# Performance work log

Hardware: AMD Instinct MI355X
Metric: run time of the kernel (lower is better)

Reference implementation:

```python
import jax, jax.numpy as jnp
import numpy as np

B, T, I, H = 64, 1024, 256, 512


def setup_inputs() -> dict:
    key = jax.random.key(0)
    ks = jax.random.split(key, 5)
    s = 1.0 / np.sqrt(H)  # PyTorch LSTM init scale (uniform(-s, s)); we use scaled normal
    return {
        "x": jax.random.normal(ks[0], (B, T, I), dtype=jnp.float32),
        "w_ih": jax.random.normal(ks[1], (4 * H, I), dtype=jnp.float32) * s,
        "w_hh": jax.random.normal(ks[2], (4 * H, H), dtype=jnp.float32) * s,
        "b_ih": jax.random.normal(ks[3], (4 * H,), dtype=jnp.float32) * s,
        "b_hh": jax.random.normal(ks[4], (4 * H,), dtype=jnp.float32) * s,
    }


def _lstm(x, w_ih, w_hh, b_ih, b_hh):
    # x: [B, T, I]. Precompute input projections for all timesteps at once.
    pre = jnp.einsum("bti,gi->btg", x, w_ih) + b_ih + b_hh  # [B, T, 4H]
    pre = jnp.swapaxes(pre, 0, 1)  # [T, B, 4H] for scan over time

    h0 = jnp.zeros((x.shape[0], H), dtype=x.dtype)
    c0 = jnp.zeros((x.shape[0], H), dtype=x.dtype)

    def step(carry, pre_t):
        h, c = carry
        gates = pre_t + h @ w_hh.T  # [B, 4H]
        i, f, g, o = jnp.split(gates, 4, axis=-1)  # PyTorch gate order: i, f, g, o
        i = jax.nn.sigmoid(i)
        f = jax.nn.sigmoid(f)
        g = jnp.tanh(g)
        o = jax.nn.sigmoid(o)
        c = f * c + i * g
        h = o * jnp.tanh(c)
        return (h, c), h

    (h_n, c_n), hs = jax.lax.scan(step, (h0, c0), pre)
    out = jnp.swapaxes(hs, 0, 1)  # [B, T, H] (batch_first=True)
    return out, (h_n[None], c_n[None])  # h_n/c_n: [num_layers=1, B, H]


def reference(x, w_ih, w_hh, b_ih, b_hh):
    return _lstm(x, w_ih, w_hh, b_ih, b_hh)
```

## Files before the change

### kernel.cpp

```cpp
#include <hip/hip_runtime.h>
#include <cstdint>
#include <cstddef>


#define NBATCH 64
#define TSTEPS 1024
#define IDIM   256
#define HDIM   512
#define WS     776
#define ABUF_USHORT (16 * WS)
#define BIAS_OFF    (2 * ABUF_USHORT * 2)
#define SMEM_BYTES  (BIAS_OFF + 1024)

#define HB_WORDS 32768

typedef __attribute__((ext_vector_type(8))) short short8x;
typedef __attribute__((ext_vector_type(4))) float f32x4;
typedef __attribute__((ext_vector_type(4))) unsigned int u32x4;

__device__ __forceinline__ float sigmoid_f(float v) {
    float e = __builtin_amdgcn_exp2f(v * -1.442695040888963f);
    return __builtin_amdgcn_rcpf(1.0f + e);
}
__device__ __forceinline__ float tanh_f(float v) {
    float e = __builtin_amdgcn_exp2f(v * 2.885390081777927f);
    return 1.0f - 2.0f * __builtin_amdgcn_rcpf(e + 1.0f);
}
__device__ __forceinline__ unsigned short f2bf(float f) {
    unsigned int u = __float_as_uint(f);
    return (unsigned short)((u + 0x7fffu + ((u >> 16) & 1u)) >> 16);
}
__device__ __forceinline__ unsigned long long pack4(float4 v) {
    unsigned long long b0 = f2bf(v.x), b1 = f2bf(v.y), b2 = f2bf(v.z), b3 = f2bf(v.w);
    return b0 | (b1 << 16) | (b2 << 32) | (b3 << 48);
}
__device__ __forceinline__ unsigned int cvtpk_bf16(float a, float b) {
    unsigned int r;
    asm("v_cvt_pk_bf16_f32 %0, %1, %2" : "=v"(r) : "v"(a), "v"(b));
    return r;
}
__device__ __forceinline__ unsigned int pklo(unsigned int a, unsigned int b) {
    return (a & 0xffffu) | (b << 16);
}
__device__ __forceinline__ float bf_lo(unsigned int w) { return __uint_as_float(w << 16); }
__device__ __forceinline__ float bf_hi(unsigned int w) { return __uint_as_float(w & 0xffff0000u); }

__global__ void __launch_bounds__(256, 1) lstm_persistent(
    const float* __restrict__ x,
    const float* __restrict__ w_ih,
    const float* __restrict__ w_hh,
    const float* __restrict__ b_ih,
    const float* __restrict__ b_hh,
    float* __restrict__ out,
    unsigned int* __restrict__ h_tb)
{
    const int tid = threadIdx.x;
    const int wg  = blockIdx.x;
    const int bg  = wg >> 3;
    const int hg  = wg & 7;

    extern __shared__ char smem[];
    unsigned short* a0 = (unsigned short*)smem;
    unsigned short* a1 = a0 + ABUF_USHORT;
    float* bias_s = (float*)(smem + BIAS_OFF);

    const int wv   = tid >> 6;
    const int lane = tid & 63;
    const int ln   = lane & 15;
    const int q    = lane >> 4;

    short8x af0[24], af1[24], af2[24], af3[24];
    {
        const int grb = (ln & 3) * HDIM + hg * 64 + wv * 16 + (ln >> 2) * 4;
#define LOADW(AF, TAU)                                                        \
        {                                                                     \
            const int gr = grb + (TAU);                                       \
            _Pragma("unroll")                                                 \
            for (int s = 0; s < 24; ++s) {                                    \
                const float* src = (s < 8)                                    \
                    ? (w_ih + (size_t)gr * IDIM + (s * 32 + q * 8))           \
                    : (w_hh + (size_t)gr * HDIM + ((s - 8) * 32 + q * 8));    \
                float4 v0 = *(const float4*)(src);                            \
                float4 v1 = *(const float4*)(src + 4);                        \
                union { short8x v; unsigned long long u[2]; } tmp;            \
                tmp.u[0] = pack4(v0);                                         \
                tmp.u[1] = pack4(v1);                                         \
                AF[s] = tmp.v;                                                \
            }                                                                 \
        }
        LOADW(af0, 0) LOADW(af1, 1) LOADW(af2, 2) LOADW(af3, 3)
#undef LOADW
    }

    if (ln < 4) {
        const int tau = ln;
        const int hid = hg * 64 + wv * 16 + q * 4 + tau;
        #pragma unroll
        for (int j = 0; j < 4; ++j)
            bias_s[(wv * 4 + q) * 16 + tau * 4 + j] =
                b_ih[j * HDIM + hid] + b_hh[j * HDIM + hid];
    }

    const int sn  = tid >> 4;
    const int sj  = tid & 15;
    const int gbn = bg * 16 + sn;
    const float* xbase = x + (size_t)gbn * TSTEPS * IDIM + sj * 16;

    const size_t hb_off = (size_t)(bg * 16 + ln) * HDIM + hg * 64 + wv * 16 + q * 4;
    float c0 = 0.f, c1 = 0.f, c2 = 0.f, c3 = 0.f;
    float hf0 = 0.f, hf1 = 0.f, hf2 = 0.f, hf3 = 0.f;

    for (int t = 0; t < TSTEPS; ++t) {
        unsigned short* abuf  = (t & 1) ? a1 : a0;
        unsigned short* axp   = abuf + sn * WS + sj * 16;
        unsigned int*   ahp32 = (unsigned int*)(abuf + sn * WS + IDIM + sj * 32);

        const float* xp = xbase + (size_t)t * IDIM;
        f32x4 xv0, xv1, xv2, xv3;
        asm volatile("global_load_dwordx4 %0, %1, off"           : "=v"(xv0) : "v"(xp));
        asm volatile("global_load_dwordx4 %0, %1, off offset:16" : "=v"(xv1) : "v"(xp));
        asm volatile("global_load_dwordx4 %0, %1, off offset:32" : "=v"(xv2) : "v"(xp));
        asm volatile("global_load_dwordx4 %0, %1, off offset:48" : "=v"(xv3) : "v"(xp));

        if (t > 0) {
            const unsigned int* hp =
                h_tb + (size_t)(t & 1) * HB_WORDS + (size_t)gbn * HDIM + sj * 32;
            u32x4 hv[8];
            const unsigned int tagw = (unsigned int)t << 16;
            unsigned pend = 0xffu;
            while (pend) {
#define POLL1(U, OFF)                                                         \
                if (pend & (1u << U))                                         \
                    asm volatile("global_load_dwordx4 %0, %1, off offset:" OFF \
                                 " sc0 sc1"                                   \
                                 : "=v"(hv[U]) : "v"(hp) : "memory");
                POLL1(0, "0")  POLL1(1, "16") POLL1(2, "32") POLL1(3, "48")
                POLL1(4, "64") POLL1(5, "80") POLL1(6, "96") POLL1(7, "112")
#undef POLL1
                asm volatile("s_waitcnt vmcnt(0)" ::: "memory");
                __builtin_amdgcn_sched_barrier(0);
                unsigned np = 0;
                #pragma unroll
                for (int u = 0; u < 8; ++u) {
                    if (pend & (1u << u)) {
                        unsigned m = ((hv[u][0] ^ tagw) | (hv[u][1] ^ tagw) |
                                      (hv[u][2] ^ tagw) | (hv[u][3] ^ tagw))
                                     & 0xffff0000u;
                        if (m) np |= (1u << u);
                    }
                }
                pend = np;
            }
            #pragma unroll
            for (int v = 0; v < 4; ++v) {
                u32x4 a = hv[2 * v], b = hv[2 * v + 1];
                u32x4 w4;
                w4[0] = pklo(a[0], a[1]);
                w4[1] = pklo(a[2], a[3]);
                w4[2] = pklo(b[0], b[1]);
                w4[3] = pklo(b[2], b[3]);
                *(u32x4*)(ahp32 + 4 * v) = w4;
            }
        } else {
            u32x4 z = {0u, 0u, 0u, 0u};
            #pragma unroll
            for (int v = 0; v < 4; ++v) *(u32x4*)(ahp32 + 4 * v) = z;
        }

        asm volatile("s_waitcnt vmcnt(0)" ::: "memory");
        __builtin_amdgcn_sched_barrier(0);
        {
            unsigned int* axp32 = (unsigned int*)axp;
            u32x4 xa, xb;
            xa[0] = cvtpk_bf16(xv0[0], xv0[1]);
            xa[1] = cvtpk_bf16(xv0[2], xv0[3]);
            xa[2] = cvtpk_bf16(xv1[0], xv1[1]);
            xa[3] = cvtpk_bf16(xv1[2], xv1[3]);
            xb[0] = cvtpk_bf16(xv2[0], xv2[1]);
            xb[1] = cvtpk_bf16(xv2[2], xv2[3]);
            xb[2] = cvtpk_bf16(xv3[0], xv3[1]);
            xb[3] = cvtpk_bf16(xv3[2], xv3[3]);
            *(u32x4*)(axp32)     = xa;
            *(u32x4*)(axp32 + 4) = xb;
        }
        __syncthreads();

        const unsigned short* Bbase = abuf + (size_t)ln * WS + q * 8;
        f32x4 ac0 = {0.f, 0.f, 0.f, 0.f};
        f32x4 ac1 = {0.f, 0.f, 0.f, 0.f};
        f32x4 ac2 = {0.f, 0.f, 0.f, 0.f};
        f32x4 ac3 = {0.f, 0.f, 0.f, 0.f};
        #pragma unroll
        for (int s = 0; s < 24; ++s) {
            short8x bf = *(const short8x*)(Bbase + s * 32);
            ac0 = __builtin_amdgcn_mfma_f32_16x16x32_bf16(af0[s], bf, ac0, 0, 0, 0);
            ac1 = __builtin_amdgcn_mfma_f32_16x16x32_bf16(af1[s], bf, ac1, 0, 0, 0);
            ac2 = __builtin_amdgcn_mfma_f32_16x16x32_bf16(af2[s], bf, ac2, 0, 0, 0);
            ac3 = __builtin_amdgcn_mfma_f32_16x16x32_bf16(af3[s], bf, ac3, 0, 0, 0);
        }

        const unsigned int tagw1 = (unsigned int)(t + 1) << 16;
        const float* bsl = bias_s + (wv * 4 + q) * 16;
        u32x4 pub;
#define ACT(ACC, TAU, CREF, HREF)                                             \
        {                                                                     \
            f32x4 bs = *(const f32x4*)(bsl + (TAU) * 4);                      \
            float ig = sigmoid_f(ACC[0] + bs[0]);                             \
            float fg = sigmoid_f(ACC[1] + bs[1]);                             \
            float gt = tanh_f   (ACC[2] + bs[2]);                             \
            float og = sigmoid_f(ACC[3] + bs[3]);                             \
            CREF = fg * CREF + ig * gt;                                       \
            HREF = og * tanh_f(CREF);                                         \
            pub[TAU] = tagw1 | (cvtpk_bf16(HREF, HREF) & 0xffffu);            \
        }
        ACT(ac0, 0, c0, hf0)
        ACT(ac1, 1, c1, hf1)
        ACT(ac2, 2, c2, hf2)
        ACT(ac3, 3, c3, hf3)
#undef ACT
        {
            unsigned int* hb = h_tb + (size_t)((t + 1) & 1) * HB_WORDS + hb_off;
            asm volatile("global_store_dwordx4 %0, %1, off sc0 sc1"
                         :: "v"(hb), "v"(pub) : "memory");
        }

        if (t > 0 && (sn & 7) == ((hg + t) & 7)) {
            float* op = out + ((size_t)gbn * TSTEPS + (t - 1)) * HDIM + sj * 32;
            #pragma unroll
            for (int v = 0; v < 4; ++v) {
                u32x4 w4 = *(const u32x4*)(ahp32 + 4 * v);
                f32x4 o0, o1;
                o0[0] = bf_lo(w4[0]); o0[1] = bf_hi(w4[0]);
                o0[2] = bf_lo(w4[1]); o0[3] = bf_hi(w4[1]);
                o1[0] = bf_lo(w4[2]); o1[1] = bf_hi(w4[2]);
                o1[2] = bf_lo(w4[3]); o1[3] = bf_hi(w4[3]);
                __builtin_nontemporal_store(o0, (f32x4*)(op + 8 * v));
                __builtin_nontemporal_store(o1, (f32x4*)(op + 8 * v + 4));
            }
        }
    }

    {
        const size_t HN_OFF = (size_t)NBATCH * TSTEPS * HDIM;
        const size_t CN_OFF = HN_OFF + (size_t)NBATCH * HDIM;
        const int gb   = bg * 16 + ln;
        const int hid0 = hg * 64 + wv * 16 + q * 4;
        f32x4 hv4 = {hf0, hf1, hf2, hf3};
        f32x4 cv4 = {c0, c1, c2, c3};
        *(f32x4*)(out + ((size_t)gb * TSTEPS + (TSTEPS - 1)) * HDIM + hid0) = hv4;
        *(f32x4*)(out + HN_OFF + (size_t)gb * HDIM + hid0) = hv4;
        *(f32x4*)(out + CN_OFF + (size_t)gb * HDIM + hid0) = cv4;
    }
}

extern "C" void kernel_launch(void* const* d_in, const int* in_sizes, int n_in,
                              void* d_out, int out_size, void* d_ws, size_t ws_size,
                              hipStream_t stream) {
    const float* x    = (const float*)d_in[0];
    const float* w_ih = (const float*)d_in[1];
    const float* w_hh = (const float*)d_in[2];
    const float* b_ih = (const float*)d_in[3];
    const float* b_hh = (const float*)d_in[4];
    float* out = (float*)d_out;

    unsigned int* h_tb = (unsigned int*)d_ws;

    (void)hipFuncSetAttribute((const void*)lstm_persistent,
                        hipFuncAttributeMaxDynamicSharedMemorySize, SMEM_BYTES);

    void* args[] = {(void*)&x, (void*)&w_ih, (void*)&w_hh, (void*)&b_ih,
                    (void*)&b_hh, (void*)&out, (void*)&h_tb};
    hipError_t err = hipLaunchCooperativeKernel((void*)lstm_persistent,
                                                dim3(32), dim3(256), args,
                                                SMEM_BYTES, stream);
    if (err != hipSuccess) {
        hipLaunchKernelGGL(lstm_persistent, dim3(32), dim3(256), SMEM_BYTES,
                           stream, x, w_ih, w_hh, b_ih, b_hh, out, h_tb);
    }
}
```

Before: 5.142 ms.

## Overlap input-projection MFMAs with hidden-state polling in persistent LSTM

Restructures each timestep so the x-projection part of the GEMM (first 8 K-slices) runs before the kernel has finished waiting for all of the previous step's hidden state from other workgroups. Hidden-state chunks that are already tagged valid are staged into LDS right away. Only the chunks that are still pending are re-polled after the x MFMAs, and a second barrier follows. This is meant to hide cross-workgroup synchronisation latency behind compute, at the cost of an extra __syncthreads per step and more complex polling control flow.

```diff
diff --git a/kernel.cpp b/kernel.cpp
--- a/kernel.cpp
+++ b/kernel.cpp
@@ -60,8 +60,8 @@
     const int hg  = wg & 7;
 
     extern __shared__ char smem[];
-    unsigned short* a0 = (unsigned short*)smem;
-    unsigned short* a1 = a0 + ABUF_USHORT;
+    unsigned short* a0s = (unsigned short*)smem;
+    unsigned short* a1s = a0s + ABUF_USHORT;
     float* bias_s = (float*)(smem + BIAS_OFF);
 
     const int wv   = tid >> 6;
@@ -111,7 +111,7 @@
     float hf0 = 0.f, hf1 = 0.f, hf2 = 0.f, hf3 = 0.f;
 
     for (int t = 0; t < TSTEPS; ++t) {
-        unsigned short* abuf  = (t & 1) ? a1 : a0;
+        unsigned short* abuf  = (t & 1) ? a1s : a0s;
         unsigned short* axp   = abuf + sn * WS + sj * 16;
         unsigned int*   ahp32 = (unsigned int*)(abuf + sn * WS + IDIM + sj * 32);
 
@@ -122,67 +122,78 @@
         asm volatile("global_load_dwordx4 %0, %1, off offset:32" : "=v"(xv2) : "v"(xp));
         asm volatile("global_load_dwordx4 %0, %1, off offset:48" : "=v"(xv3) : "v"(xp));
 
+        unsigned pend = 0;
+        u32x4 hv[8];
+        const unsigned int tagw = (unsigned int)t << 16;
+        const unsigned int* hp =
+            h_tb + (size_t)(t & 1) * HB_WORDS + (size_t)gbn * HDIM + sj * 32;
+
+#define POLL1(U, OFF)                                                         \
+        if (pend & (1u << U))                                                 \
+            asm volatile("global_load_dwordx4 %0, %1, off offset:" OFF        \
+                         " sc0 sc1"                                           \
+                         : "=v"(hv[U]) : "v"(hp) : "memory");
+#define CHECKSTAGE(U)                                                         \
+        if (pend & (1u << U)) {                                               \
+            unsigned m = ((hv[U][0] ^ tagw) | (hv[U][1] ^ tagw) |             \
+                          (hv[U][2] ^ tagw) | (hv[U][3] ^ tagw))              \
+                         & 0xffff0000u;                                       \
+            if (!m) {                                                         \
+                unsigned int p0 = pklo(hv[U][0], hv[U][1]);                   \
+                unsigned int p1 = pklo(hv[U][2], hv[U][3]);                   \
+                unsigned long long pw = (unsigned long long)p0                \
+                                      | ((unsigned long long)p1 << 32);       \
+                *(unsigned long long*)(ahp32 + 2 * (U)) = pw;                 \
+                pend &= ~(1u << U);                                           \
+            }                                                                 \
+        }
+
         if (t > 0) {
-            const unsigned int* hp =
-                h_tb + (size_t)(t & 1) * HB_WORDS + (size_t)gbn * HDIM + sj * 32;
-            u32x4 hv[8];
-            const unsigned int tagw = (unsigned int)t << 16;
-            unsigned pend = 0xffu;
-            while (pend) {
-#define POLL1(U, OFF)                                                         \
-                if (pend & (1u << U))                                         \
-                    asm volatile("global_load_dwordx4 %0, %1, off offset:" OFF \
-                                 " sc0 sc1"                                   \
-                                 : "=v"(hv[U]) : "v"(hp) : "memory");
-                POLL1(0, "0")  POLL1(1, "16") POLL1(2, "32") POLL1(3, "48")
-                POLL1(4, "64") POLL1(5, "80") POLL1(6, "96") POLL1(7, "112")
-#undef POLL1
-                asm volatile("s_waitcnt vmcnt(0)" ::: "memory");
-                __builtin_amdgcn_sched_barrier(0);
-                unsigned np = 0;
-                #pragma unroll
-                for (int u = 0; u < 8; ++u) {
-                    if (pend & (1u << u)) {
-                        unsigned m = ((hv[u][0] ^ tagw) | (hv[u][1] ^ tagw) |
-                                      (hv[u][2] ^ tagw) | (hv[u][3] ^ tagw))
-                                     & 0xffff0000u;
-                        if (m) np |= (1u << u);
-                    }
-                }
-                pend = np;
+            pend = 0xffu;
+            POLL1(0, "0")  POLL1(1, "16") POLL1(2, "32") POLL1(3, "48")
+            POLL1(4, "64") POLL1(5, "80") POLL1(6, "96") POLL1(7, "112")
+            asm volatile("s_waitcnt vmcnt(4)" ::: "memory");
+            __builtin_amdgcn_sched_barrier(0);
+            {
+                unsigned int* axp32 = (unsigned int*)axp;
+                u32x4 xa, xb;
+                xa[0] = cvtpk_bf16(xv0[0], xv0[1]);
+                xa[1] = cvtpk_bf16(xv0[2], xv0[3]);
+                xa[2] = cvtpk_bf16(xv1[0], xv1[1]);
+                xa[3] = cvtpk_bf16(xv1[2], xv1[3]);
+                xb[0] = cvtpk_bf16(xv2[0], xv2[1]);
+                xb[1] = cvtpk_bf16(xv2[2], xv2[3]);
+                xb[2] = cvtpk_bf16(xv3[0], xv3[1]);
+                xb[3] = cvtpk_bf16(xv3[2], xv3[3]);
+                *(u32x4*)(axp32)     = xa;
+                *(u32x4*)(axp32 + 4) = xb;
             }
-            #pragma unroll
-            for (int v = 0; v < 4; ++v) {
-                u32x4 a = hv[2 * v], b = hv[2 * v + 1];
-                u32x4 w4;
-                w4[0] = pklo(a[0], a[1]);
-                w4[1] = pklo(a[2], a[3]);
-                w4[2] = pklo(b[0], b[1]);
-                w4[3] = pklo(b[2], b[3]);
-                *(u32x4*)(ahp32 + 4 * v) = w4;
+            CHECKSTAGE(0) CHECKSTAGE(1) CHECKSTAGE(2) CHECKSTAGE(3)
+            asm volatile("s_waitcnt vmcnt(0)" ::: "memory");
+            __builtin_amdgcn_sched_barrier(0);
+            CHECKSTAGE(4) CHECKSTAGE(5) CHECKSTAGE(6) CHECKSTAGE(7)
+        } else {
+            asm volatile("s_waitcnt vmcnt(0)" ::: "memory");
+            __builtin_amdgcn_sched_barrier(0);
+            {
+                unsigned int* axp32 = (unsigned int*)axp;
+                u32x4 xa, xb;
+                xa[0] = cvtpk_bf16(xv0[0], xv0[1]);
+                xa[1] = cvtpk_bf16(xv0[2], xv0[3]);
+                xa[2] = cvtpk_bf16(xv1[0], xv1[1]);
+                xa[3] = cvtpk_bf16(xv1[2], xv1[3]);
+                xb[0] = cvtpk_bf16(xv2[0], xv2[1]);
+                xb[1] = cvtpk_bf16(xv2[2], xv2[3]);
+                xb[2] = cvtpk_bf16(xv3[0], xv3[1]);
+                xb[3] = cvtpk_bf16(xv3[2], xv3[3]);
+                *(u32x4*)(axp32)     = xa;
+                *(u32x4*)(axp32 + 4) = xb;
             }
-        } else {
             u32x4 z = {0u, 0u, 0u, 0u};
             #pragma unroll
             for (int v = 0; v < 4; ++v) *(u32x4*)(ahp32 + 4 * v) = z;
         }
 
-        asm volatile("s_waitcnt vmcnt(0)" ::: "memory");
-        __builtin_amdgcn_sched_barrier(0);
-        {
-            unsigned int* axp32 = (unsigned int*)axp;
-            u32x4 xa, xb;
-            xa[0] = cvtpk_bf16(xv0[0], xv0[1]);
-            xa[1] = cvtpk_bf16(xv0[2], xv0[3]);
-            xa[2] = cvtpk_bf16(xv1[0], xv1[1]);
-            xa[3] = cvtpk_bf16(xv1[2], xv1[3]);
-            xb[0] = cvtpk_bf16(xv2[0], xv2[1]);
-            xb[1] = cvtpk_bf16(xv2[2], xv2[3]);
-            xb[2] = cvtpk_bf16(xv3[0], xv3[1]);
-            xb[3] = cvtpk_bf16(xv3[2], xv3[3]);
-            *(u32x4*)(axp32)     = xa;
-            *(u32x4*)(axp32 + 4) = xb;
-        }
         __syncthreads();
 
         const unsigned short* Bbase = abuf + (size_t)ln * WS + q * 8;
@@ -191,7 +202,27 @@
         f32x4 ac2 = {0.f, 0.f, 0.f, 0.f};
         f32x4 ac3 = {0.f, 0.f, 0.f, 0.f};
         #pragma unroll
-        for (int s = 0; s < 24; ++s) {
+        for (int s = 0; s < 8; ++s) {
+            short8x bf = *(const short8x*)(Bbase + s * 32);
+            ac0 = __builtin_amdgcn_mfma_f32_16x16x32_bf16(af0[s], bf, ac0, 0, 0, 0);
+            ac1 = __builtin_amdgcn_mfma_f32_16x16x32_bf16(af1[s], bf, ac1, 0, 0, 0);
+            ac2 = __builtin_amdgcn_mfma_f32_16x16x32_bf16(af2[s], bf, ac2, 0, 0, 0);
+            ac3 = __builtin_amdgcn_mfma_f32_16x16x32_bf16(af3[s], bf, ac3, 0, 0, 0);
+        }
+
+        while (pend) {
+            POLL1(0, "0")  POLL1(1, "16") POLL1(2, "32") POLL1(3, "48")
+            POLL1(4, "64") POLL1(5, "80") POLL1(6, "96") POLL1(7, "112")
+            asm volatile("s_waitcnt vmcnt(0)" ::: "memory");
+            __builtin_amdgcn_sched_barrier(0);
+            CHECKSTAGE(0) CHECKSTAGE(1) CHECKSTAGE(2) CHECKSTAGE(3)
+            CHECKSTAGE(4) CHECKSTAGE(5) CHECKSTAGE(6) CHECKSTAGE(7)
+        }
+
+        __syncthreads();
+
+        #pragma unroll
+        for (int s = 8; s < 24; ++s) {
             short8x bf = *(const short8x*)(Bbase + s * 32);
             ac0 = __builtin_amdgcn_mfma_f32_16x16x32_bf16(af0[s], bf, ac0, 0, 0, 0);
             ac1 = __builtin_amdgcn_mfma_f32_16x16x32_bf16(af1[s], bf, ac1, 0, 0, 0);
@@ -238,6 +269,8 @@
                 __builtin_nontemporal_store(o1, (f32x4*)(op + 8 * v + 4));
             }
         }
+#undef POLL1
+#undef CHECKSTAGE
     }
 
     {
```

Result: slower. 5.808 ms (+13.0%).
